# Performance work log

Hardware: AMD Instinct MI355X
Metric: run time of the kernel (lower is better)

Reference implementation:

```python
import jax, jax.numpy as jnp
import numpy as np

N = 100000        # nodes
E = 1600000       # directed edges (avg degree 16)
F_IN, F_HID, F_OUT = 512, 32, 16


def setup_inputs() -> dict:
    key = jax.random.key(0)
    k0, k1, k2, k3 = jax.random.split(key, 4)
    x = jax.random.normal(k0, (N, F_IN), dtype=jnp.float32)
    edge_index = jax.random.randint(k1, (2, E), 0, N, dtype=jnp.int32)
    # Glorot-ish init for the two GCNConv linear weights
    W1 = jax.random.normal(k2, (F_IN, F_HID), dtype=jnp.float32) / np.float32(np.sqrt(F_IN))
    W2 = jax.random.normal(k3, (F_HID, F_OUT), dtype=jnp.float32) / np.float32(np.sqrt(F_HID))
    b1 = jnp.zeros((F_HID,), jnp.float32)
    b2 = jnp.zeros((F_OUT,), jnp.float32)
    return {"x": x, "W1": W1, "b1": b1, "W2": W2, "b2": b2, "edge_index": edge_index}


def gcn_conv(x, W, b, src, dst):
    """PyG GCNConv: h = x W; symmetric-normalized aggregation with self-loops; + bias."""
    h = x @ W                                   # [N, F_out] project first (PyG order)
    # degree including the implicit self-loop (start from ones)
    deg = jnp.ones((N,), h.dtype).at[dst].add(1.0)
    dinv = jax.lax.rsqrt(deg)                   # deg^{-1/2}
    coef = (dinv[src] * dinv[dst])[:, None]     # [E, 1] edge norm
    msg = h[src] * coef                         # gather + scale
    agg = jax.ops.segment_sum(msg, dst, num_segments=N)  # scatter-add to dst
    agg = agg + h * (dinv * dinv)[:, None]      # self-loop contribution
    return agg + b


def reference(x, W1, b1, W2, b2, edge_index):
    src, dst = edge_index[0], edge_index[1]
    h = jax.nn.relu(gcn_conv(x, W1, b1, src, dst))
    # F.dropout(training=self.training) is identity in eval mode
    h = gcn_conv(h, W2, b2, src, dst)
    return jax.nn.log_softmax(h, axis=1)
```

## Files before the change

kernel.cpp:

```cpp
#include <hip/hip_runtime.h>
#include <hip/hip_bf16.h>
#include <cstdint>

#define NN   100000
#define NE   1600000
#define FIN  512
#define FHID 32
#define FOUT 16

#define BSHIFT 8
#define BSIZE  256
#define NBUCK  391
#define EPB    2048
#define NCHUNK ((NE + EPB - 1) / EPB)

typedef float f32x4 __attribute__((ext_vector_type(4)));
typedef short s16x8 __attribute__((ext_vector_type(8)));
typedef short s16x4 __attribute__((ext_vector_type(4)));
typedef int   i32x4 __attribute__((ext_vector_type(4)));
typedef unsigned int u32;
typedef unsigned short u16;

__device__ __forceinline__ short f2bf(float f) {
  union { float f; uint32_t u; } v; v.f = f;
  uint32_t r = v.u + 0x7fffu + ((v.u >> 16) & 1u);
  return (short)(r >> 16);
}
__device__ __forceinline__ float bf2f(u16 u) {
  union { uint32_t u; float f; } v; v.u = (uint32_t)u << 16; return v.f;
}

__global__ __launch_bounds__(256) void k_hist(const int* __restrict__ dst,
                                              u32* __restrict__ bcount) {
  __shared__ u32 h[NBUCK];
  int tid = threadIdx.x;
  for (int i = tid; i < NBUCK; i += 256) h[i] = 0;
  __syncthreads();
  int base = blockIdx.x * EPB;
  #pragma unroll
  for (int i = 0; i < 2; ++i) {
    int e0 = base + (i * 256 + tid) * 4;
    if (e0 + 3 < NE) {
      i32x4 d4 = *(const i32x4*)(dst + e0);
      atomicAdd(&h[d4[0] >> BSHIFT], 1u);
      atomicAdd(&h[d4[1] >> BSHIFT], 1u);
      atomicAdd(&h[d4[2] >> BSHIFT], 1u);
      atomicAdd(&h[d4[3] >> BSHIFT], 1u);
    } else {
      for (int k = 0; k < 4; ++k)
        if (e0 + k < NE) atomicAdd(&h[dst[e0 + k] >> BSHIFT], 1u);
    }
  }
  __syncthreads();
  for (int i = tid; i < NBUCK; i += 256)
    if (h[i]) atomicAdd(&bcount[i], h[i]);
}

__global__ __launch_bounds__(512) void k_bscan(const u32* __restrict__ bc,
                                               u32* __restrict__ bstart,
                                               u32* __restrict__ bcur) {
  __shared__ u32 tmp[512];
  int tid = threadIdx.x;
  u32 v = (tid < NBUCK) ? bc[tid] : 0;
  tmp[tid] = v;
  __syncthreads();
  #pragma unroll
  for (int off = 1; off < 512; off <<= 1) {
    u32 t = (tid >= off) ? tmp[tid - off] : 0;
    __syncthreads();
    tmp[tid] += t;
    __syncthreads();
  }
  if (tid < NBUCK) { u32 e = tmp[tid] - v; bstart[tid] = e; bcur[tid] = e; }
  if (tid == 511) bstart[NBUCK] = tmp[511];
}

__global__ __launch_bounds__(512) void k_bin(const int* __restrict__ src,
                                             const int* __restrict__ dst,
                                             u32* __restrict__ bcur,
                                             u32* __restrict__ binned) {
  __shared__ u32 cnt[NBUCK];
  __shared__ u32 lofs[NBUCK];
  __shared__ u32 gbase[NBUCK];
  __shared__ u32 tmp[512];
  __shared__ u32 stage[EPB];
  __shared__ u16 sb[EPB];
  int tid = threadIdx.x;
  for (int i = tid; i < NBUCK; i += 512) cnt[i] = 0;
  __syncthreads();

  int base = blockIdx.x * EPB;
  int e0 = base + tid * 4;
  u32 vals[4];
  u32 ofs[4];
  int bks[4];
  if (e0 + 3 < NE) {
    i32x4 s4 = *(const i32x4*)(src + e0);
    i32x4 d4 = *(const i32x4*)(dst + e0);
    #pragma unroll
    for (int k = 0; k < 4; ++k) {
      int b = d4[k] >> BSHIFT;
      bks[k] = b;
      vals[k] = (u32)s4[k] | ((u32)(d4[k] & (BSIZE - 1)) << 17);
      ofs[k] = atomicAdd(&cnt[b], 1u);
    }
  } else {
    #pragma unroll
    for (int k = 0; k < 4; ++k) {
      int e = e0 + k;
      bool ok = e < NE;
      int s = 0, d = 0;
      if (ok) { s = src[e]; d = dst[e]; }
      int b = ok ? (d >> BSHIFT) : -1;
      bks[k] = b;
      vals[k] = (u32)s | ((u32)(d & (BSIZE - 1)) << 17);
      ofs[k] = ok ? atomicAdd(&cnt[b], 1u) : 0;
    }
  }
  __syncthreads();

  u32 cv = (tid < NBUCK) ? cnt[tid] : 0;
  tmp[tid] = cv;
  __syncthreads();
  #pragma unroll
  for (int off = 1; off < 512; off <<= 1) {
    u32 t = (tid >= off) ? tmp[tid - off] : 0;
    __syncthreads();
    tmp[tid] += t;
    __syncthreads();
  }
  if (tid < NBUCK) {
    lofs[tid] = tmp[tid] - cv;
    gbase[tid] = cv ? atomicAdd(&bcur[tid], cv) : 0;
  }
  __syncthreads();
  u32 total = tmp[511];
  __syncthreads();

  #pragma unroll
  for (int k = 0; k < 4; ++k) {
    if (bks[k] >= 0) {
      u32 sl = lofs[bks[k]] + ofs[k];
      stage[sl] = vals[k];
      sb[sl] = (u16)bks[k];
    }
  }
  __syncthreads();

  for (u32 s2 = tid; s2 < total; s2 += 512) {
    int b = sb[s2];
    binned[gbase[b] + (s2 - lofs[b])] = stage[s2];
  }
}

__global__ __launch_bounds__(256) void k_fin(const u32* __restrict__ binned,
                                             const u32* __restrict__ bstart,
                                             int* __restrict__ deg,
                                             int* __restrict__ rs,
                                             float* __restrict__ dinv,
                                             int* __restrict__ csr) {
  __shared__ u32 degl[BSIZE];
  __shared__ u32 rsl[BSIZE];
  int tid = threadIdx.x;
  int b = blockIdx.x;
  u32 start = bstart[b];
  u32 n = bstart[b + 1] - start;

  degl[tid] = 0;
  __syncthreads();
  for (u32 k = tid; k < n; k += 256)
    atomicAdd(&degl[binned[start + k] >> 17], 1u);
  __syncthreads();

  u32 v = degl[tid];
  rsl[tid] = v;
  __syncthreads();
  #pragma unroll
  for (int off = 1; off < 256; off <<= 1) {
    u32 t = (tid >= off) ? rsl[tid - off] : 0;
    __syncthreads();
    rsl[tid] += t;
    __syncthreads();
  }
  u32 e = rsl[tid] - v;
  __syncthreads();
  rsl[tid] = e;

  int g = b * BSIZE + tid;
  if (g < NN) {
    deg[g] = (int)v;
    rs[g] = (int)(start + e);
    dinv[g] = rsqrtf(1.0f + (float)v);
  }
  __syncthreads();

  for (u32 k = tid; k < n; k += 256) {
    u32 vv = binned[start + k];
    u32 pos = atomicAdd(&rsl[vv >> 17], 1u);
    csr[start + pos] = (int)(vv & 0x1FFFFu);
  }
}

__global__ __launch_bounds__(256) void k_gemm1(const float* __restrict__ x,
                                               const float* __restrict__ W1,
                                               const float* __restrict__ dinv,
                                               u16* __restrict__ Hs1) {
  __shared__ s16x8 Blds[16][2][64];
  const int tid = threadIdx.x;
  for (int it = 0; it < 64; ++it) {
    int flat = it * 256 + tid;
    int i  = flat & 7;
    int l  = (flat >> 3) & 63;
    int nt = (flat >> 9) & 1;
    int kt = flat >> 10;
    int k  = kt * 32 + ((l >> 4) << 3) + i;
    int n  = nt * 16 + (l & 15);
    ((short*)Blds)[flat] = f2bf(W1[k * 32 + n]);
  }
  __syncthreads();

  const int lane = tid & 63;
  const int wv   = tid >> 6;
  const int h    = lane >> 4;
  const int m    = lane & 15;
  const int wid  = blockIdx.x * 4 + wv;
  if (wid >= 3125) return;
  const int t0 = wid * 2;

  const float* xr0 = x + (size_t)(t0 * 16 + m) * FIN + h * 8;
  const float* xr1 = xr0 + (size_t)16 * FIN;

  f32x4 acc[2][2] = {};
  #pragma unroll
  for (int kt = 0; kt < 16; ++kt) {
    f32x4 a0 = *(const f32x4*)(xr0 + kt * 32);
    f32x4 a1 = *(const f32x4*)(xr0 + kt * 32 + 4);
    f32x4 c0 = *(const f32x4*)(xr1 + kt * 32);
    f32x4 c1 = *(const f32x4*)(xr1 + kt * 32 + 4);
    s16x8 b0 = Blds[kt][0][lane];
    s16x8 b1 = Blds[kt][1][lane];
    s16x8 af, cf;
    af[0]=f2bf(a0[0]); af[1]=f2bf(a0[1]); af[2]=f2bf(a0[2]); af[3]=f2bf(a0[3]);
    af[4]=f2bf(a1[0]); af[5]=f2bf(a1[1]); af[6]=f2bf(a1[2]); af[7]=f2bf(a1[3]);
    cf[0]=f2bf(c0[0]); cf[1]=f2bf(c0[1]); cf[2]=f2bf(c0[2]); cf[3]=f2bf(c0[3]);
    cf[4]=f2bf(c1[0]); cf[5]=f2bf(c1[1]); cf[6]=f2bf(c1[2]); cf[7]=f2bf(c1[3]);
    acc[0][0] = __builtin_amdgcn_mfma_f32_16x16x32_bf16(af, b0, acc[0][0], 0, 0, 0);
    acc[0][1] = __builtin_amdgcn_mfma_f32_16x16x32_bf16(af, b1, acc[0][1], 0, 0, 0);
    acc[1][0] = __builtin_amdgcn_mfma_f32_16x16x32_bf16(cf, b0, acc[1][0], 0, 0, 0);
    acc[1][1] = __builtin_amdgcn_mfma_f32_16x16x32_bf16(cf, b1, acc[1][1], 0, 0, 0);
  }
  #pragma unroll
  for (int rt = 0; rt < 2; ++rt) {
    #pragma unroll
    for (int r = 0; r < 4; ++r) {
      int row = (t0 + rt) * 16 + h * 4 + r;
      float di = dinv[row];
      u16* o = Hs1 + (size_t)row * FHID + m;
      o[0]  = (u16)f2bf(acc[rt][0][r] * di);
      o[16] = (u16)f2bf(acc[rt][1][r] * di);
    }
  }
}

__global__ __launch_bounds__(256) void k_gat1(const int* __restrict__ csr,
                                              const int* __restrict__ rs,
                                              const int* __restrict__ deg,
                                              const float* __restrict__ dinv,
                                              const float* __restrict__ b1,
                                              const float* __restrict__ W2,
                                              const u16* __restrict__ Hs1,
                                              u16* __restrict__ Hs2) {
  __shared__ float w[FHID * FOUT];
  for (int i = threadIdx.x; i < FHID * FOUT; i += 256) w[i] = W2[i];
  __syncthreads();

  int t = blockIdx.x * 256 + threadIdx.x;
  int d = t >> 2;
  if (d >= NN) return;
  int p = t & 3;
  int start = rs[d], n = deg[d];

  float a0[8], a1[8], a2[8], a3[8];
  {
    s16x8 v = *(const s16x8*)(Hs1 + (size_t)d * FHID + p * 8);
    #pragma unroll
    for (int k = 0; k < 8; ++k) {
      a0[k] = bf2f((u16)v[k]); a1[k] = 0.f; a2[k] = 0.f; a3[k] = 0.f;
    }
  }
  int j = 0;
  for (; j + 8 <= n; j += 8) {
    int s0 = csr[start + j];
    int s1 = csr[start + j + 1];
    int s2 = csr[start + j + 2];
    int s3 = csr[start + j + 3];
    int s4 = csr[start + j + 4];
    int s5 = csr[start + j + 5];
    int s6 = csr[start + j + 6];
    int s7 = csr[start + j + 7];
    s16x8 v0 = *(const s16x8*)(Hs1 + (size_t)s0 * FHID + p * 8);
    s16x8 v1 = *(const s16x8*)(Hs1 + (size_t)s1 * FHID + p * 8);
    s16x8 v2 = *(const s16x8*)(Hs1 + (size_t)s2 * FHID + p * 8);
    s16x8 v3 = *(const s16x8*)(Hs1 + (size_t)s3 * FHID + p * 8);
    s16x8 v4 = *(const s16x8*)(Hs1 + (size_t)s4 * FHID + p * 8);
    s16x8 v5 = *(const s16x8*)(Hs1 + (size_t)s5 * FHID + p * 8);
    s16x8 v6 = *(const s16x8*)(Hs1 + (size_t)s6 * FHID + p * 8);
    s16x8 v7 = *(const s16x8*)(Hs1 + (size_t)s7 * FHID + p * 8);
    #pragma unroll
    for (int k = 0; k < 8; ++k) {
      a0[k] += bf2f((u16)v0[k]);
      a1[k] += bf2f((u16)v1[k]);
      a2[k] += bf2f((u16)v2[k]);
      a3[k] += bf2f((u16)v3[k]);
      a0[k] += bf2f((u16)v4[k]);
      a1[k] += bf2f((u16)v5[k]);
      a2[k] += bf2f((u16)v6[k]);
      a3[k] += bf2f((u16)v7[k]);
    }
  }
  for (; j + 4 <= n; j += 4) {
    int s0 = csr[start + j];
    int s1 = csr[start + j + 1];
    int s2 = csr[start + j + 2];
    int s3 = csr[start + j + 3];
    s16x8 v0 = *(const s16x8*)(Hs1 + (size_t)s0 * FHID + p * 8);
    s16x8 v1 = *(const s16x8*)(Hs1 + (size_t)s1 * FHID + p * 8);
    s16x8 v2 = *(const s16x8*)(Hs1 + (size_t)s2 * FHID + p * 8);
    s16x8 v3 = *(const s16x8*)(Hs1 + (size_t)s3 * FHID + p * 8);
    #pragma unroll
    for (int k = 0; k < 8; ++k) {
      a0[k] += bf2f((u16)v0[k]);
      a1[k] += bf2f((u16)v1[k]);
      a2[k] += bf2f((u16)v2[k]);
      a3[k] += bf2f((u16)v3[k]);
    }
  }
  for (; j < n; ++j) {
    int s0 = csr[start + j];
    s16x8 v0 = *(const s16x8*)(Hs1 + (size_t)s0 * FHID + p * 8);
    #pragma unroll
    for (int k = 0; k < 8; ++k) a0[k] += bf2f((u16)v0[k]);
  }

  float dd = dinv[d];
  float h[8];
  #pragma unroll
  for (int k = 0; k < 8; ++k)
    h[k] = fmaxf(((a0[k] + a1[k]) + (a2[k] + a3[k])) * dd + b1[p * 8 + k], 0.0f);

  float pj[FOUT];
  #pragma unroll
  for (int jj = 0; jj < FOUT; ++jj) pj[jj] = 0.f;
  #pragma unroll
  for (int k = 0; k < 8; ++k)
    #pragma unroll
    for (int jj = 0; jj < FOUT; ++jj)
      pj[jj] = fmaf(h[k], w[(p * 8 + k) * FOUT + jj], pj[jj]);
  #pragma unroll
  for (int jj = 0; jj < FOUT; ++jj) {
    pj[jj] += __shfl_xor(pj[jj], 1);
    pj[jj] += __shfl_xor(pj[jj], 2);
  }
  s16x4 o;
  #pragma unroll
  for (int q = 0; q < 4; ++q) o[q] = f2bf(pj[p * 4 + q] * dd);
  *(s16x4*)(Hs2 + (size_t)d * FOUT + p * 4) = o;
}

__global__ __launch_bounds__(256) void k_gat2(const int* __restrict__ csr,
                                              const int* __restrict__ rs,
                                              const int* __restrict__ deg,
                                              const float* __restrict__ dinv,
                                              const float* __restrict__ b2,
                                              const u16* __restrict__ Hs2,
                                              float* __restrict__ out) {
  int t = blockIdx.x * 256 + threadIdx.x;
  int d = t >> 2;
  if (d >= NN) return;
  int p = t & 3;
  int start = rs[d], n = deg[d];

  float a0[4], a1[4], a2[4], a3[4];
  {
    s16x4 v = *(const s16x4*)(Hs2 + (size_t)d * FOUT + p * 4);
    #pragma unroll
    for (int k = 0; k < 4; ++k) {
      a0[k] = bf2f((u16)v[k]); a1[k] = 0.f; a2[k] = 0.f; a3[k] = 0.f;
    }
  }
  int j = 0;
  for (; j + 8 <= n; j += 8) {
    int s0 = csr[start + j];
    int s1 = csr[start + j + 1];
    int s2 = csr[start + j + 2];
    int s3 = csr[start + j + 3];
    int s4 = csr[start + j + 4];
    int s5 = csr[start + j + 5];
    int s6 = csr[start + j + 6];
    int s7 = csr[start + j + 7];
    s16x4 v0 = *(const s16x4*)(Hs2 + (size_t)s0 * FOUT + p * 4);
    s16x4 v1 = *(const s16x4*)(Hs2 + (size_t)s1 * FOUT + p * 4);
    s16x4 v2 = *(const s16x4*)(Hs2 + (size_t)s2 * FOUT + p * 4);
    s16x4 v3 = *(const s16x4*)(Hs2 + (size_t)s3 * FOUT + p * 4);
    s16x4 v4 = *(const s16x4*)(Hs2 + (size_t)s4 * FOUT + p * 4);
    s16x4 v5 = *(const s16x4*)(Hs2 + (size_t)s5 * FOUT + p * 4);
    s16x4 v6 = *(const s16x4*)(Hs2 + (size_t)s6 * FOUT + p * 4);
    s16x4 v7 = *(const s16x4*)(Hs2 + (size_t)s7 * FOUT + p * 4);
    #pragma unroll
    for (int k = 0; k < 4; ++k) {
      a0[k] += bf2f((u16)v0[k]);
      a1[k] += bf2f((u16)v1[k]);
      a2[k] += bf2f((u16)v2[k]);
      a3[k] += bf2f((u16)v3[k]);
      a0[k] += bf2f((u16)v4[k]);
      a1[k] += bf2f((u16)v5[k]);
      a2[k] += bf2f((u16)v6[k]);
      a3[k] += bf2f((u16)v7[k]);
    }
  }
  for (; j + 4 <= n; j += 4) {
    int s0 = csr[start + j];
    int s1 = csr[start + j + 1];
    int s2 = csr[start + j + 2];
    int s3 = csr[start + j + 3];
    s16x4 v0 = *(const s16x4*)(Hs2 + (size_t)s0 * FOUT + p * 4);
    s16x4 v1 = *(const s16x4*)(Hs2 + (size_t)s1 * FOUT + p * 4);
    s16x4 v2 = *(const s16x4*)(Hs2 + (size_t)s2 * FOUT + p * 4);
    s16x4 v3 = *(const s16x4*)(Hs2 + (size_t)s3 * FOUT + p * 4);
    #pragma unroll
    for (int k = 0; k < 4; ++k) {
      a0[k] += bf2f((u16)v0[k]);
      a1[k] += bf2f((u16)v1[k]);
      a2[k] += bf2f((u16)v2[k]);
      a3[k] += bf2f((u16)v3[k]);
    }
  }
  for (; j < n; ++j) {
    int s0 = csr[start + j];
    s16x4 v0 = *(const s16x4*)(Hs2 + (size_t)s0 * FOUT + p * 4);
    #pragma unroll
    for (int k = 0; k < 4; ++k) a0[k] += bf2f((u16)v0[k]);
  }

  float dd = dinv[d];
  float z[4];
  #pragma unroll
  for (int k = 0; k < 4; ++k)
    z[k] = ((a0[k] + a1[k]) + (a2[k] + a3[k])) * dd + b2[p * 4 + k];

  float m = fmaxf(fmaxf(z[0], z[1]), fmaxf(z[2], z[3]));
  m = fmaxf(m, __shfl_xor(m, 1));
  m = fmaxf(m, __shfl_xor(m, 2));
  float s = expf(z[0]-m) + expf(z[1]-m) + expf(z[2]-m) + expf(z[3]-m);
  s += __shfl_xor(s, 1);
  s += __shfl_xor(s, 2);
  float lse = m + logf(s);

  f32x4 o = { z[0]-lse, z[1]-lse, z[2]-lse, z[3]-lse };
  *(f32x4*)(out + (size_t)d * FOUT + p * 4) = o;
}

extern "C" void kernel_launch(void* const* d_in, const int* in_sizes, int n_in,
                              void* d_out, int out_size, void* d_ws, size_t ws_size,
                              hipStream_t stream) {
  const float* x  = (const float*)d_in[0];
  const float* W1 = (const float*)d_in[1];
  const float* b1 = (const float*)d_in[2];
  const float* W2 = (const float*)d_in[3];
  const float* b2 = (const float*)d_in[4];
  const int*   ei = (const int*)d_in[5];
  const int* srcv = ei;
  const int* dstv = ei + NE;

  char* ws = (char*)d_ws;
  const size_t KB = 1024, MB = 1048576;
  u32*   bcount = (u32*)(ws + 0);
  u32*   bstart = (u32*)(ws + 8 * KB);
  u32*   bcur   = (u32*)(ws + 16 * KB);
  int*   deg    = (int*)(ws + 512 * KB);
  int*   rs     = (int*)(ws + 1024 * KB);
  float* dinv   = (float*)(ws + 1536 * KB);
  u32*   binned = (u32*)(ws + 2 * MB);
  int*   csr    = (int*)(ws + 9 * MB);
  u16*   Hs1    = (u16*)(ws + 16 * MB);
  u16*   Hs2    = (u16*)(ws + 23 * MB);
  float* out    = (float*)d_out;

  hipMemsetAsync(bcount, 0, NBUCK * sizeof(u32), stream);

  k_hist <<<NCHUNK, 256, 0, stream>>>(dstv, bcount);
  k_bscan<<<1,      512, 0, stream>>>(bcount, bstart, bcur);
  k_bin  <<<NCHUNK, 512, 0, stream>>>(srcv, dstv, bcur, binned);
  k_fin  <<<NBUCK,  256, 0, stream>>>(binned, bstart, deg, rs, dinv, csr);
  k_gemm1<<<782, 256, 0, stream>>>(x, W1, dinv, Hs1);
  k_gat1 <<<(NN * 4 + 255) / 256, 256, 0, stream>>>(csr, rs, deg, dinv, b1, W2, Hs1, Hs2);
  k_gat2 <<<(NN * 4 + 255) / 256, 256, 0, stream>>>(csr, rs, deg, dinv, b2, Hs2, out);
}
```

Measured before the change: 164.3 us.

## Fuse CSR build phases with layer-1 GEMM in one persistent kernel

```diff
diff --git a/kernel.cpp b/kernel.cpp
--- a/kernel.cpp
+++ b/kernel.cpp
@@ -8,11 +8,14 @@
 #define FHID 32
 #define FOUT 16
 
-#define BSHIFT 8
-#define BSIZE  256
-#define NBUCK  391
-#define EPB    2048
-#define NCHUNK ((NE + EPB - 1) / EPB)
+#define BSHIFT 9
+#define BSIZE  512
+#define NBUCK  196
+#define CPB    1024
+#define NCHUNK ((NE + CPB - 1) / CPB)
+#define NCSR   192
+#define GEMMB  782
+#define TOTB   (NCSR + GEMMB)
 
 typedef float f32x4 __attribute__((ext_vector_type(4)));
 typedef short s16x8 __attribute__((ext_vector_type(8)));
@@ -30,183 +33,200 @@
   union { uint32_t u; float f; } v; v.u = (uint32_t)u << 16; return v.f;
 }
 
-__global__ __launch_bounds__(256) void k_hist(const int* __restrict__ dst,
-                                              u32* __restrict__ bcount) {
-  __shared__ u32 h[NBUCK];
-  int tid = threadIdx.x;
-  for (int i = tid; i < NBUCK; i += 256) h[i] = 0;
-  __syncthreads();
-  int base = blockIdx.x * EPB;
-  #pragma unroll
-  for (int i = 0; i < 2; ++i) {
-    int e0 = base + (i * 256 + tid) * 4;
-    if (e0 + 3 < NE) {
-      i32x4 d4 = *(const i32x4*)(dst + e0);
-      atomicAdd(&h[d4[0] >> BSHIFT], 1u);
-      atomicAdd(&h[d4[1] >> BSHIFT], 1u);
-      atomicAdd(&h[d4[2] >> BSHIFT], 1u);
-      atomicAdd(&h[d4[3] >> BSHIFT], 1u);
+struct BinSh {
+  u32 cnt[NBUCK]; u32 lofs[NBUCK]; u32 gbase[NBUCK]; u32 tmp[256];
+  u32 stage[CPB]; u16 sb[CPB];
+};
+struct FinSh { u32 degl[BSIZE]; u32 rsl[BSIZE]; u32 tmp[256]; };
+union ShU {
+  s16x8 B[16][2][64];
+  u32 hist[NBUCK];
+  u32 scan[256];
+  BinSh bin;
+  FinSh fin;
+};
+
+__global__ __launch_bounds__(256) void k_fused(
+    const int* __restrict__ src, const int* __restrict__ dst,
+    const float* __restrict__ x, const float* __restrict__ W1,
+    u32* __restrict__ bcount, u32* __restrict__ ph,
+    u32* __restrict__ bstart, u32* __restrict__ bcur,
+    int* __restrict__ deg, int* __restrict__ rs, float* __restrict__ dinv,
+    int* __restrict__ csr, u32* __restrict__ binned,
+    u16* __restrict__ H1) {
+  __shared__ ShU sh;
+  const int tid = threadIdx.x;
+
+  if (blockIdx.x < NCSR) {
+    const int cb = blockIdx.x;
+
+    for (int i = tid; i < NBUCK; i += 256) sh.hist[i] = 0;
+    __syncthreads();
+    for (int c = cb; c < NCHUNK; c += NCSR) {
+      int e0 = c * CPB + tid * 4;
+      if (e0 + 3 < NE) {
+        i32x4 d4 = *(const i32x4*)(dst + e0);
+        atomicAdd(&sh.hist[d4[0] >> BSHIFT], 1u);
+        atomicAdd(&sh.hist[d4[1] >> BSHIFT], 1u);
+        atomicAdd(&sh.hist[d4[2] >> BSHIFT], 1u);
+        atomicAdd(&sh.hist[d4[3] >> BSHIFT], 1u);
+      } else {
+        for (int k = 0; k < 4; ++k)
+          if (e0 + k < NE) atomicAdd(&sh.hist[dst[e0 + k] >> BSHIFT], 1u);
+      }
+    }
+    __syncthreads();
+    for (int i = tid; i < NBUCK; i += 256)
+      if (sh.hist[i]) atomicAdd(&bcount[i], sh.hist[i]);
+    __syncthreads();
+    if (tid == 0)
+      __hip_atomic_fetch_add(&ph[0], 1u, __ATOMIC_ACQ_REL, __HIP_MEMORY_SCOPE_AGENT);
+
+    if (cb == 0) {
+      if (tid == 0)
+        while (__hip_atomic_load(&ph[0], __ATOMIC_ACQUIRE, __HIP_MEMORY_SCOPE_AGENT) < NCSR)
+          __builtin_amdgcn_s_sleep(2);
+      __syncthreads();
+      u32 v = (tid < NBUCK) ? bcount[tid] : 0;
+      sh.scan[tid] = v;
+      __syncthreads();
+      #pragma unroll
+      for (int off = 1; off < 256; off <<= 1) {
+        u32 t = (tid >= off) ? sh.scan[tid - off] : 0;
+        __syncthreads();
+        sh.scan[tid] += t;
+        __syncthreads();
+      }
+      if (tid < NBUCK) {
+        u32 e = sh.scan[tid] - v;
+        bstart[tid] = e;
+        bcur[tid] = e;
+      }
+      if (tid == 255) bstart[NBUCK] = sh.scan[255];
+      __syncthreads();
+      if (tid == 0)
+        __hip_atomic_store(&ph[1], 1u, __ATOMIC_RELEASE, __HIP_MEMORY_SCOPE_AGENT);
     } else {
-      for (int k = 0; k < 4; ++k)
-        if (e0 + k < NE) atomicAdd(&h[dst[e0 + k] >> BSHIFT], 1u);
-    }
-  }
-  __syncthreads();
-  for (int i = tid; i < NBUCK; i += 256)
-    if (h[i]) atomicAdd(&bcount[i], h[i]);
-}
-
-__global__ __launch_bounds__(512) void k_bscan(const u32* __restrict__ bc,
-                                               u32* __restrict__ bstart,
-                                               u32* __restrict__ bcur) {
-  __shared__ u32 tmp[512];
-  int tid = threadIdx.x;
-  u32 v = (tid < NBUCK) ? bc[tid] : 0;
-  tmp[tid] = v;
-  __syncthreads();
-  #pragma unroll
-  for (int off = 1; off < 512; off <<= 1) {
-    u32 t = (tid >= off) ? tmp[tid - off] : 0;
+      if (tid == 0)
+        while (__hip_atomic_load(&ph[1], __ATOMIC_ACQUIRE, __HIP_MEMORY_SCOPE_AGENT) < 1)
+          __builtin_amdgcn_s_sleep(2);
+      __syncthreads();
+    }
+
+    for (int c = cb; c < NCHUNK; c += NCSR) {
+      for (int i = tid; i < NBUCK; i += 256) sh.bin.cnt[i] = 0;
+      __syncthreads();
+      int e0 = c * CPB + tid * 4;
+      u32 vals[4]; u32 ofs[4]; int bks[4];
+      if (e0 + 3 < NE) {
+        i32x4 s4 = *(const i32x4*)(src + e0);
+        i32x4 d4 = *(const i32x4*)(dst + e0);
+        #pragma unroll
+        for (int k = 0; k < 4; ++k) {
+          int b = d4[k] >> BSHIFT;
+          bks[k] = b;
+          vals[k] = (u32)s4[k] | ((u32)(d4[k] & (BSIZE - 1)) << 17);
+          ofs[k] = atomicAdd(&sh.bin.cnt[b], 1u);
+        }
+      } else {
+        #pragma unroll
+        for (int k = 0; k < 4; ++k) {
+          int e = e0 + k;
+          bool ok = e < NE;
+          int s = 0, d = 0;
+          if (ok) { s = src[e]; d = dst[e]; }
+          int b = ok ? (d >> BSHIFT) : -1;
+          bks[k] = b;
+          vals[k] = (u32)s | ((u32)(d & (BSIZE - 1)) << 17);
+          ofs[k] = ok ? atomicAdd(&sh.bin.cnt[b], 1u) : 0;
+        }
+      }
+      __syncthreads();
+      u32 cv = (tid < NBUCK) ? sh.bin.cnt[tid] : 0;
+      sh.bin.tmp[tid] = cv;
+      __syncthreads();
+      #pragma unroll
+      for (int off = 1; off < 256; off <<= 1) {
+        u32 t = (tid >= off) ? sh.bin.tmp[tid - off] : 0;
+        __syncthreads();
+        sh.bin.tmp[tid] += t;
+        __syncthreads();
+      }
+      if (tid < NBUCK) {
+        sh.bin.lofs[tid] = sh.bin.tmp[tid] - cv;
+        sh.bin.gbase[tid] = cv ? atomicAdd(&bcur[tid], cv) : 0;
+      }
+      __syncthreads();
+      u32 total = sh.bin.tmp[255];
+      __syncthreads();
+      #pragma unroll
+      for (int k = 0; k < 4; ++k) {
+        if (bks[k] >= 0) {
+          u32 sl = sh.bin.lofs[bks[k]] + ofs[k];
+          sh.bin.stage[sl] = vals[k];
+          sh.bin.sb[sl] = (u16)bks[k];
+        }
+      }
+      __syncthreads();
+      for (u32 s2 = tid; s2 < total; s2 += 256) {
+        int b = sh.bin.sb[s2];
+        binned[sh.bin.gbase[b] + (s2 - sh.bin.lofs[b])] = sh.bin.stage[s2];
+      }
+      __syncthreads();
+    }
+    if (tid == 0) {
+      __hip_atomic_fetch_add(&ph[2], 1u, __ATOMIC_ACQ_REL, __HIP_MEMORY_SCOPE_AGENT);
+      while (__hip_atomic_load(&ph[2], __ATOMIC_ACQUIRE, __HIP_MEMORY_SCOPE_AGENT) < NCSR)
+        __builtin_amdgcn_s_sleep(2);
+    }
     __syncthreads();
-    tmp[tid] += t;
-    __syncthreads();
-  }
-  if (tid < NBUCK) { u32 e = tmp[tid] - v; bstart[tid] = e; bcur[tid] = e; }
-  if (tid == 511) bstart[NBUCK] = tmp[511];
-}
-
-__global__ __launch_bounds__(512) void k_bin(const int* __restrict__ src,
-                                             const int* __restrict__ dst,
-                                             u32* __restrict__ bcur,
-                                             u32* __restrict__ binned) {
-  __shared__ u32 cnt[NBUCK];
-  __shared__ u32 lofs[NBUCK];
-  __shared__ u32 gbase[NBUCK];
-  __shared__ u32 tmp[512];
-  __shared__ u32 stage[EPB];
-  __shared__ u16 sb[EPB];
-  int tid = threadIdx.x;
-  for (int i = tid; i < NBUCK; i += 512) cnt[i] = 0;
-  __syncthreads();
-
-  int base = blockIdx.x * EPB;
-  int e0 = base + tid * 4;
-  u32 vals[4];
-  u32 ofs[4];
-  int bks[4];
-  if (e0 + 3 < NE) {
-    i32x4 s4 = *(const i32x4*)(src + e0);
-    i32x4 d4 = *(const i32x4*)(dst + e0);
-    #pragma unroll
-    for (int k = 0; k < 4; ++k) {
-      int b = d4[k] >> BSHIFT;
-      bks[k] = b;
-      vals[k] = (u32)s4[k] | ((u32)(d4[k] & (BSIZE - 1)) << 17);
-      ofs[k] = atomicAdd(&cnt[b], 1u);
-    }
-  } else {
-    #pragma unroll
-    for (int k = 0; k < 4; ++k) {
-      int e = e0 + k;
-      bool ok = e < NE;
-      int s = 0, d = 0;
-      if (ok) { s = src[e]; d = dst[e]; }
-      int b = ok ? (d >> BSHIFT) : -1;
-      bks[k] = b;
-      vals[k] = (u32)s | ((u32)(d & (BSIZE - 1)) << 17);
-      ofs[k] = ok ? atomicAdd(&cnt[b], 1u) : 0;
-    }
-  }
-  __syncthreads();
-
-  u32 cv = (tid < NBUCK) ? cnt[tid] : 0;
-  tmp[tid] = cv;
-  __syncthreads();
-  #pragma unroll
-  for (int off = 1; off < 512; off <<= 1) {
-    u32 t = (tid >= off) ? tmp[tid - off] : 0;
-    __syncthreads();
-    tmp[tid] += t;
-    __syncthreads();
-  }
-  if (tid < NBUCK) {
-    lofs[tid] = tmp[tid] - cv;
-    gbase[tid] = cv ? atomicAdd(&bcur[tid], cv) : 0;
-  }
-  __syncthreads();
-  u32 total = tmp[511];
-  __syncthreads();
-
-  #pragma unroll
-  for (int k = 0; k < 4; ++k) {
-    if (bks[k] >= 0) {
-      u32 sl = lofs[bks[k]] + ofs[k];
-      stage[sl] = vals[k];
-      sb[sl] = (u16)bks[k];
-    }
-  }
-  __syncthreads();
-
-  for (u32 s2 = tid; s2 < total; s2 += 512) {
-    int b = sb[s2];
-    binned[gbase[b] + (s2 - lofs[b])] = stage[s2];
-  }
-}
-
-__global__ __launch_bounds__(256) void k_fin(const u32* __restrict__ binned,
-                                             const u32* __restrict__ bstart,
-                                             int* __restrict__ deg,
-                                             int* __restrict__ rs,
-                                             float* __restrict__ dinv,
-                                             int* __restrict__ csr) {
-  __shared__ u32 degl[BSIZE];
-  __shared__ u32 rsl[BSIZE];
-  int tid = threadIdx.x;
-  int b = blockIdx.x;
-  u32 start = bstart[b];
-  u32 n = bstart[b + 1] - start;
-
-  degl[tid] = 0;
-  __syncthreads();
-  for (u32 k = tid; k < n; k += 256)
-    atomicAdd(&degl[binned[start + k] >> 17], 1u);
-  __syncthreads();
-
-  u32 v = degl[tid];
-  rsl[tid] = v;
-  __syncthreads();
-  #pragma unroll
-  for (int off = 1; off < 256; off <<= 1) {
-    u32 t = (tid >= off) ? rsl[tid - off] : 0;
-    __syncthreads();
-    rsl[tid] += t;
-    __syncthreads();
-  }
-  u32 e = rsl[tid] - v;
-  __syncthreads();
-  rsl[tid] = e;
-
-  int g = b * BSIZE + tid;
-  if (g < NN) {
-    deg[g] = (int)v;
-    rs[g] = (int)(start + e);
-    dinv[g] = rsqrtf(1.0f + (float)v);
-  }
-  __syncthreads();
-
-  for (u32 k = tid; k < n; k += 256) {
-    u32 vv = binned[start + k];
-    u32 pos = atomicAdd(&rsl[vv >> 17], 1u);
-    csr[start + pos] = (int)(vv & 0x1FFFFu);
-  }
-}
-
-__global__ __launch_bounds__(256) void k_gemm1(const float* __restrict__ x,
-                                               const float* __restrict__ W1,
-                                               const float* __restrict__ dinv,
-                                               u16* __restrict__ Hs1) {
-  __shared__ s16x8 Blds[16][2][64];
-  const int tid = threadIdx.x;
+
+    for (int b = cb; b < NBUCK; b += NCSR) {
+      u32 start = bstart[b];
+      u32 n = bstart[b + 1] - start;
+      sh.fin.degl[tid] = 0; sh.fin.degl[tid + 256] = 0;
+      __syncthreads();
+      for (u32 k = tid; k < n; k += 256)
+        atomicAdd(&sh.fin.degl[binned[start + k] >> 17], 1u);
+      __syncthreads();
+      u32 a0 = sh.fin.degl[2 * tid], a1 = sh.fin.degl[2 * tid + 1];
+      u32 s = a0 + a1;
+      sh.fin.tmp[tid] = s;
+      __syncthreads();
+      #pragma unroll
+      for (int off = 1; off < 256; off <<= 1) {
+        u32 t = (tid >= off) ? sh.fin.tmp[tid - off] : 0;
+        __syncthreads();
+        sh.fin.tmp[tid] += t;
+        __syncthreads();
+      }
+      u32 e = sh.fin.tmp[tid] - s;
+      sh.fin.rsl[2 * tid] = e;
+      sh.fin.rsl[2 * tid + 1] = e + a0;
+      __syncthreads();
+      #pragma unroll
+      for (int q = 0; q < 2; ++q) {
+        int t = tid + q * 256;
+        int g = b * BSIZE + t;
+        if (g < NN) {
+          u32 dg = sh.fin.degl[t];
+          deg[g] = (int)dg;
+          rs[g] = (int)(start + sh.fin.rsl[t]);
+          dinv[g] = rsqrtf(1.0f + (float)dg);
+        }
+      }
+      __syncthreads();
+      for (u32 k = tid; k < n; k += 256) {
+        u32 vv = binned[start + k];
+        u32 pos = atomicAdd(&sh.fin.rsl[vv >> 17], 1u);
+        csr[start + pos] = (int)(vv & 0x1FFFFu);
+      }
+      __syncthreads();
+    }
+    return;
+  }
+
+  const int bid = blockIdx.x - NCSR;
   for (int it = 0; it < 64; ++it) {
     int flat = it * 256 + tid;
     int i  = flat & 7;
@@ -215,7 +235,7 @@
     int kt = flat >> 10;
     int k  = kt * 32 + ((l >> 4) << 3) + i;
     int n  = nt * 16 + (l & 15);
-    ((short*)Blds)[flat] = f2bf(W1[k * 32 + n]);
+    ((short*)sh.B)[flat] = f2bf(W1[k * 32 + n]);
   }
   __syncthreads();
 
@@ -223,7 +243,7 @@
   const int wv   = tid >> 6;
   const int h    = lane >> 4;
   const int m    = lane & 15;
-  const int wid  = blockIdx.x * 4 + wv;
+  const int wid  = bid * 4 + wv;
   if (wid >= 3125) return;
   const int t0 = wid * 2;
 
@@ -237,8 +257,8 @@
     f32x4 a1 = *(const f32x4*)(xr0 + kt * 32 + 4);
     f32x4 c0 = *(const f32x4*)(xr1 + kt * 32);
     f32x4 c1 = *(const f32x4*)(xr1 + kt * 32 + 4);
-    s16x8 b0 = Blds[kt][0][lane];
-    s16x8 b1 = Blds[kt][1][lane];
+    s16x8 b0 = sh.B[kt][0][lane];
+    s16x8 b1 = sh.B[kt][1][lane];
     s16x8 af, cf;
     af[0]=f2bf(a0[0]); af[1]=f2bf(a0[1]); af[2]=f2bf(a0[2]); af[3]=f2bf(a0[3]);
     af[4]=f2bf(a1[0]); af[5]=f2bf(a1[1]); af[6]=f2bf(a1[2]); af[7]=f2bf(a1[3]);
@@ -254,10 +274,9 @@
     #pragma unroll
     for (int r = 0; r < 4; ++r) {
       int row = (t0 + rt) * 16 + h * 4 + r;
-      float di = dinv[row];
-      u16* o = Hs1 + (size_t)row * FHID + m;
-      o[0]  = (u16)f2bf(acc[rt][0][r] * di);
-      o[16] = (u16)f2bf(acc[rt][1][r] * di);
+      u16* o = H1 + (size_t)row * FHID + m;
+      o[0]  = (u16)f2bf(acc[rt][0][r]);
+      o[16] = (u16)f2bf(acc[rt][1][r]);
     }
   }
 }
@@ -268,7 +287,7 @@
                                               const float* __restrict__ dinv,
                                               const float* __restrict__ b1,
                                               const float* __restrict__ W2,
-                                              const u16* __restrict__ Hs1,
+                                              const u16* __restrict__ H1,
                                               u16* __restrict__ Hs2) {
   __shared__ float w[FHID * FOUT];
   for (int i = threadIdx.x; i < FHID * FOUT; i += 256) w[i] = W2[i];
@@ -279,13 +298,14 @@
   if (d >= NN) return;
   int p = t & 3;
   int start = rs[d], n = deg[d];
+  float dd = dinv[d];
 
   float a0[8], a1[8], a2[8], a3[8];
   {
-    s16x8 v = *(const s16x8*)(Hs1 + (size_t)d * FHID + p * 8);
+    s16x8 v = *(const s16x8*)(H1 + (size_t)d * FHID + p * 8);
     #pragma unroll
     for (int k = 0; k < 8; ++k) {
-      a0[k] = bf2f((u16)v[k]); a1[k] = 0.f; a2[k] = 0.f; a3[k] = 0.f;
+      a0[k] = dd * bf2f((u16)v[k]); a1[k] = 0.f; a2[k] = 0.f; a3[k] = 0.f;
     }
   }
   int j = 0;
@@ -298,24 +318,26 @@
     int s5 = csr[start + j + 5];
     int s6 = csr[start + j + 6];
     int s7 = csr[start + j + 7];
-    s16x8 v0 = *(const s16x8*)(Hs1 + (size_t)s0 * FHID + p * 8);
-    s16x8 v1 = *(const s16x8*)(Hs1 + (size_t)s1 * FHID + p * 8);
-    s16x8 v2 = *(const s16x8*)(Hs1 + (size_t)s2 * FHID + p * 8);
-    s16x8 v3 = *(const s16x8*)(Hs1 + (size_t)s3 * FHID + p * 8);
-    s16x8 v4 = *(const s16x8*)(Hs1 + (size_t)s4 * FHID + p * 8);
-    s16x8 v5 = *(const s16x8*)(Hs1 + (size_t)s5 * FHID + p * 8);
-    s16x8 v6 = *(const s16x8*)(Hs1 + (size_t)s6 * FHID + p * 8);
-    s16x8 v7 = *(const s16x8*)(Hs1 + (size_t)s7 * FHID + p * 8);
+    float d0 = dinv[s0], d1 = dinv[s1], d2 = dinv[s2], d3 = dinv[s3];
+    float d4 = dinv[s4], d5 = dinv[s5], d6 = dinv[s6], d7 = dinv[s7];
+    s16x8 v0 = *(const s16x8*)(H1 + (size_t)s0 * FHID + p * 8);
+    s16x8 v1 = *(const s16x8*)(H1 + (size_t)s1 * FHID + p * 8);
+    s16x8 v2 = *(const s16x8*)(H1 + (size_t)s2 * FHID + p * 8);
+    s16x8 v3 = *(const s16x8*)(H1 + (size_t)s3 * FHID + p * 8);
+    s16x8 v4 = *(const s16x8*)(H1 + (size_t)s4 * FHID + p * 8);
+    s16x8 v5 = *(const s16x8*)(H1 + (size_t)s5 * FHID + p * 8);
+    s16x8 v6 = *(const s16x8*)(H1 + (size_t)s6 * FHID + p * 8);
+    s16x8 v7 = *(const s16x8*)(H1 + (size_t)s7 * FHID + p * 8);
     #pragma unroll
     for (int k = 0; k < 8; ++k) {
-      a0[k] += bf2f((u16)v0[k]);
-      a1[k] += bf2f((u16)v1[k]);
-      a2[k] += bf2f((u16)v2[k]);
-      a3[k] += bf2f((u16)v3[k]);
-      a0[k] += bf2f((u16)v4[k]);
-      a1[k] += bf2f((u16)v5[k]);
-      a2[k] += bf2f((u16)v6[k]);
-      a3[k] += bf2f((u16)v7[k]);
+      a0[k] = fmaf(d0, bf2f((u16)v0[k]), a0[k]);
+      a1[k] = fmaf(d1, bf2f((u16)v1[k]), a1[k]);
+      a2[k] = fmaf(d2, bf2f((u16)v2[k]), a2[k]);
+      a3[k] = fmaf(d3, bf2f((u16)v3[k]), a3[k]);
+      a0[k] = fmaf(d4, bf2f((u16)v4[k]), a0[k]);
+      a1[k] = fmaf(d5, bf2f((u16)v5[k]), a1[k]);
+      a2[k] = fmaf(d6, bf2f((u16)v6[k]), a2[k]);
+      a3[k] = fmaf(d7, bf2f((u16)v7[k]), a3[k]);
     }
   }
   for (; j + 4 <= n; j += 4) {
@@ -323,26 +345,27 @@
     int s1 = csr[start + j + 1];
     int s2 = csr[start + j + 2];
     int s3 = csr[start + j + 3];
-    s16x8 v0 = *(const s16x8*)(Hs1 + (size_t)s0 * FHID + p * 8);
-    s16x8 v1 = *(const s16x8*)(Hs1 + (size_t)s1 * FHID + p * 8);
-    s16x8 v2 = *(const s16x8*)(Hs1 + (size_t)s2 * FHID + p * 8);
-    s16x8 v3 = *(const s16x8*)(Hs1 + (size_t)s3 * FHID + p * 8);
+    float d0 = dinv[s0], d1 = dinv[s1], d2 = dinv[s2], d3 = dinv[s3];
+    s16x8 v0 = *(const s16x8*)(H1 + (size_t)s0 * FHID + p * 8);
+    s16x8 v1 = *(const s16x8*)(H1 + (size_t)s1 * FHID + p * 8);
+    s16x8 v2 = *(const s16x8*)(H1 + (size_t)s2 * FHID + p * 8);
+    s16x8 v3 = *(const s16x8*)(H1 + (size_t)s3 * FHID + p * 8);
     #pragma unroll
     for (int k = 0; k < 8; ++k) {
-      a0[k] += bf2f((u16)v0[k]);
-      a1[k] += bf2f((u16)v1[k]);
-      a2[k] += bf2f((u16)v2[k]);
-      a3[k] += bf2f((u16)v3[k]);
+      a0[k] = fmaf(d0, bf2f((u16)v0[k]), a0[k]);
+      a1[k] = fmaf(d1, bf2f((u16)v1[k]), a1[k]);
+      a2[k] = fmaf(d2, bf2f((u16)v2[k]), a2[k]);
+      a3[k] = fmaf(d3, bf2f((u16)v3[k]), a3[k]);
     }
   }
   for (; j < n; ++j) {
     int s0 = csr[start + j];
-    s16x8 v0 = *(const s16x8*)(Hs1 + (size_t)s0 * FHID + p * 8);
-    #pragma unroll
-    for (int k = 0; k < 8; ++k) a0[k] += bf2f((u16)v0[k]);
-  }
-
-  float dd = dinv[d];
+    float d0 = dinv[s0];
+    s16x8 v0 = *(const s16x8*)(H1 + (size_t)s0 * FHID + p * 8);
+    #pragma unroll
+    for (int k = 0; k < 8; ++k) a0[k] = fmaf(d0, bf2f((u16)v0[k]), a0[k]);
+  }
+
   float h[8];
   #pragma unroll
   for (int k = 0; k < 8; ++k)
@@ -475,6 +498,7 @@
   char* ws = (char*)d_ws;
   const size_t KB = 1024, MB = 1048576;
   u32*   bcount = (u32*)(ws + 0);
+  u32*   ph     = (u32*)(ws + 1 * KB);
   u32*   bstart = (u32*)(ws + 8 * KB);
   u32*   bcur   = (u32*)(ws + 16 * KB);
   int*   deg    = (int*)(ws + 512 * KB);
@@ -482,17 +506,14 @@
   float* dinv   = (float*)(ws + 1536 * KB);
   u32*   binned = (u32*)(ws + 2 * MB);
   int*   csr    = (int*)(ws + 9 * MB);
-  u16*   Hs1    = (u16*)(ws + 16 * MB);
+  u16*   H1     = (u16*)(ws + 16 * MB);
   u16*   Hs2    = (u16*)(ws + 23 * MB);
   float* out    = (float*)d_out;
 
-  hipMemsetAsync(bcount, 0, NBUCK * sizeof(u32), stream);
-
-  k_hist <<<NCHUNK, 256, 0, stream>>>(dstv, bcount);
-  k_bscan<<<1,      512, 0, stream>>>(bcount, bstart, bcur);
-  k_bin  <<<NCHUNK, 512, 0, stream>>>(srcv, dstv, bcur, binned);
-  k_fin  <<<NBUCK,  256, 0, stream>>>(binned, bstart, deg, rs, dinv, csr);
-  k_gemm1<<<782, 256, 0, stream>>>(x, W1, dinv, Hs1);
-  k_gat1 <<<(NN * 4 + 255) / 256, 256, 0, stream>>>(csr, rs, deg, dinv, b1, W2, Hs1, Hs2);
+  hipMemsetAsync(ws, 0, 2 * KB, stream);
+
+  k_fused<<<TOTB, 256, 0, stream>>>(srcv, dstv, x, W1, bcount, ph,
+                                    bstart, bcur, deg, rs, dinv, csr, binned, H1);
+  k_gat1 <<<(NN * 4 + 255) / 256, 256, 0, stream>>>(csr, rs, deg, dinv, b1, W2, H1, Hs2);
   k_gat2 <<<(NN * 4 + 255) / 256, 256, 0, stream>>>(csr, rs, deg, dinv, b2, Hs2, out);
 }
```

Result: slower. 182.3 us (+11.0%).
